# Performance work log

Hardware: AMD Instinct MI355X
Metric: run time of the kernel (lower is better)

## Reference

```python
import jax, jax.numpy as jnp
import numpy as np
import math

B, S, D, H, DFF = 4, 1024, 1024, 16, 4096
DK = D // H
EPS = 1e-6


def setup_inputs() -> dict:
    key = jax.random.key(0)
    ks = jax.random.split(key, 8)
    sc = 1.0 / math.sqrt(D)
    return {
        "x": jax.random.normal(ks[0], (B, S, D), jnp.float32),
        "src_mask": jnp.ones((B, 1, 1, S), jnp.int32),
        "wq": jax.random.normal(ks[1], (D, D), jnp.float32) * sc,
        "bq": jnp.zeros((D,), jnp.float32),
        "wk": jax.random.normal(ks[2], (D, D), jnp.float32) * sc,
        "bk": jnp.zeros((D,), jnp.float32),
        "wv": jax.random.normal(ks[3], (D, D), jnp.float32) * sc,
        "bv": jnp.zeros((D,), jnp.float32),
        "wo": jax.random.normal(ks[4], (D, D), jnp.float32) * sc,
        "bo": jnp.zeros((D,), jnp.float32),
        "w1": jax.random.normal(ks[5], (D, DFF), jnp.float32) * sc,
        "b1": jnp.zeros((DFF,), jnp.float32),
        "w2": jax.random.normal(ks[6], (DFF, D), jnp.float32) * (1.0 / math.sqrt(DFF)),
        "b2": jnp.zeros((D,), jnp.float32),
        "alpha1": jnp.ones((1,), jnp.float32),
        "beta1": jnp.zeros((1,), jnp.float32),
        "alpha2": jnp.ones((1,), jnp.float32),
        "beta2": jnp.zeros((1,), jnp.float32),
    }


def layer_norm(x, alpha, beta):
    # Faithful to the custom LayerNormalization: scalar alpha/beta,
    # torch std (unbiased, ddof=1), eps added to std (not variance).
    mean = jnp.mean(x, axis=-1, keepdims=True)
    std = jnp.std(x, axis=-1, keepdims=True, ddof=1)
    return alpha * (x - mean) / (std + EPS) + beta


def encoder_block(x, src_mask, wq, bq, wk, bk, wv, bv, wo, bo,
                  w1, b1, w2, b2, alpha1, beta1, alpha2, beta2):
    # --- residual 1: pre-norm self-attention (dropout = 0 / eval mode) ---
    xn = layer_norm(x, alpha1, beta1)
    q = (xn @ wq + bq).reshape(B, S, H, DK).transpose(0, 2, 1, 3)  # bhsd
    k = (xn @ wk + bk).reshape(B, S, H, DK).transpose(0, 2, 1, 3)
    v = (xn @ wv + bv).reshape(B, S, H, DK).transpose(0, 2, 1, 3)
    scores = jnp.einsum("bhqd,bhkd->bhqk", q, k) / math.sqrt(DK)
    scores = jnp.where(src_mask == 0, jnp.float32(-1e9), scores)
    attn = jax.nn.softmax(scores, axis=-1)
    ctx = jnp.einsum("bhqk,bhkd->bhqd", attn, v)
    ctx = ctx.transpose(0, 2, 1, 3).reshape(B, S, D)
    x = x + (ctx @ wo + bo)
    # --- residual 2: pre-norm feed-forward ---
    xn2 = layer_norm(x, alpha2, beta2)
    ff = jax.nn.relu(xn2 @ w1 + b1) @ w2 + b2
    return x + ff


def reference(x, src_mask, wq, bq, wk, bk, wv, bv, wo, bo,
              w1, b1, w2, b2, alpha1, beta1, alpha2, beta2):
    return encoder_block(x, src_mask, wq, bq, wk, bk, wv, bv, wo, bo,
                         w1, b1, w2, b2, alpha1, beta1, alpha2, beta2)
```

## Files before the change

kernel.cpp:

```cpp
#include <hip/hip_runtime.h>
#include <hip/hip_bf16.h>
#include <stdint.h>


typedef unsigned short u16;
typedef __attribute__((ext_vector_type(4))) float f32x4;
typedef __attribute__((ext_vector_type(8))) short bf16x8;
typedef __attribute__((ext_vector_type(4))) unsigned short u16x4;

__device__ __forceinline__ u16 f2b(float f) {
  unsigned int u = __builtin_bit_cast(unsigned int, f);
  u += 0x7FFFu + ((u >> 16) & 1u);
  return (u16)(u >> 16);
}

__device__ __forceinline__ void gload_lds16(const void* g, void* l) {
  __builtin_amdgcn_global_load_lds(
      reinterpret_cast<__attribute__((address_space(1))) void*>(
          reinterpret_cast<uintptr_t>(g)),
      reinterpret_cast<__attribute__((address_space(3))) void*>(
          reinterpret_cast<uintptr_t>(l)),
      16, 0, 0);
}

#define MFMA16(a, b, c) __builtin_amdgcn_mfma_f32_16x16x32_bf16((a), (b), (c), 0, 0, 0)

__global__ __launch_bounds__(256) void cast_transpose(
    const float* __restrict__ in, u16* __restrict__ out, int K, int N) {
  __shared__ float tile[32][33];
  const int n0 = blockIdx.x * 32, k0 = blockIdx.y * 32;
  const int tx = threadIdx.x & 31, ty = threadIdx.x >> 5;
#pragma unroll
  for (int i = 0; i < 32; i += 8)
    tile[ty + i][tx] = in[(int64_t)(k0 + ty + i) * N + (n0 + tx)];
  __syncthreads();
#pragma unroll
  for (int i = 0; i < 32; i += 8)
    out[(int64_t)(n0 + ty + i) * K + (k0 + tx)] = f2b(tile[tx][ty + i]);
}

__global__ void pack_bias(const float* __restrict__ bq, const float* __restrict__ bk,
                          const float* __restrict__ bv, float* __restrict__ out) {
  int i = blockIdx.x * 256 + threadIdx.x;
  const float* src = (i < 1024) ? bq : (i < 2048 ? bk : bv);
  out[i] = src[i & 1023];
}

__global__ __launch_bounds__(256) void transpose_v(
    const u16* __restrict__ qkv, u16* __restrict__ vt) {
  __shared__ u16 t[32][33];
  const int bh = blockIdx.z;
  const int b = bh >> 4, h = bh & 15;
  const int s0 = blockIdx.x * 32, d0 = blockIdx.y * 32;
  const int tx = threadIdx.x & 31, ty = threadIdx.x >> 5;
  const u16* src = qkv + (int64_t)(b * 1024) * 3072 + 2048 + h * 64;
#pragma unroll
  for (int i = 0; i < 32; i += 8)
    t[ty + i][tx] = src[(int64_t)(s0 + ty + i) * 3072 + d0 + tx];
  __syncthreads();
  u16* dst = vt + (int64_t)bh * 64 * 1024;
#pragma unroll
  for (int i = 0; i < 32; i += 8)
    dst[(int64_t)(d0 + ty + i) * 1024 + s0 + tx] = t[tx][ty + i];
}

__global__ __launch_bounds__(256) void layernorm_k(
    const float* __restrict__ x, const float* __restrict__ alpha,
    const float* __restrict__ beta, u16* __restrict__ out) {
  const int row = blockIdx.x;
  const float4 v = ((const float4*)(x + (int64_t)row * 1024))[threadIdx.x];
  float s = v.x + v.y + v.z + v.w;
  float sq = v.x * v.x + v.y * v.y + v.z * v.z + v.w * v.w;
#pragma unroll
  for (int off = 1; off < 64; off <<= 1) {
    s += __shfl_xor(s, off, 64);
    sq += __shfl_xor(sq, off, 64);
  }
  __shared__ float ss[4], ssq[4];
  const int wid = threadIdx.x >> 6;
  if ((threadIdx.x & 63) == 0) { ss[wid] = s; ssq[wid] = sq; }
  __syncthreads();
  s = ss[0] + ss[1] + ss[2] + ss[3];
  sq = ssq[0] + ssq[1] + ssq[2] + ssq[3];
  const float mean = s * (1.0f / 1024.0f);
  float var = (sq - 1024.0f * mean * mean) * (1.0f / 1023.0f);
  var = fmaxf(var, 0.0f);
  const float inv = alpha[0] / (sqrtf(var) + 1e-6f);
  const float bt = beta[0];
  u16x4 o;
  o[0] = f2b((v.x - mean) * inv + bt);
  o[1] = f2b((v.y - mean) * inv + bt);
  o[2] = f2b((v.z - mean) * inv + bt);
  o[3] = f2b((v.w - mean) * inv + bt);
  *(u16x4*)(out + (int64_t)row * 1024 + threadIdx.x * 4) = o;
}

template <int BN, bool OUT_BF16, bool RELU, bool RES>
__global__ __launch_bounds__(256) void gemm_bt(
    const u16* __restrict__ A, const u16* __restrict__ Bt,
    const float* __restrict__ bias, const float* __restrict__ res,
    void* __restrict__ Cout, int Ndim, int K) {
  constexpr int NF = BN / 32;
  __shared__ u16 Alds[2][128 * 32];
  __shared__ u16 Blds[2][BN * 32];
  const int tid = threadIdx.x;
  const int wid = tid >> 6, lane = tid & 63;
  int flat = blockIdx.y * gridDim.x + blockIdx.x;
  const int cpx = (gridDim.x * gridDim.y) >> 3;
  flat = (flat & 7) * cpx + (flat >> 3);
  const int bm0 = (flat / gridDim.x) * 128;
  const int bn0 = (flat % gridDim.x) * BN;
  const int wm = (wid >> 1) * 64, wn = (wid & 1) * (BN / 2);
  const int lrow = lane & 15, lg = lane >> 4;

  f32x4 acc[4][NF] = {};

  const int srow = tid >> 2, skoff = (tid & 3) * 8;
  const u16* Ag = A + (int64_t)(bm0 + srow) * K + skoff;
  const u16* Bg = Bt + (int64_t)(bn0 + srow) * K + skoff;
  const int64_t half = (int64_t)64 * K;

  auto stage = [&](int buf) {
    char* ad = (char*)&Alds[buf][0] + tid * 16;
    char* bd = (char*)&Blds[buf][0] + tid * 16;
    gload_lds16(Ag, ad);
    gload_lds16(Ag + half, ad + 4096);
    gload_lds16(Bg, bd);
    if (BN == 128) gload_lds16(Bg + half, bd + 4096);
    Ag += 32; Bg += 32;
  };

  const int nK = K >> 5;
  stage(0);
  __syncthreads();
  int cur = 0;
  for (int kt = 0; kt < nK; ++kt) {
    if (kt + 1 < nK) stage(cur ^ 1);
    bf16x8 af[4], bfr[NF];
#pragma unroll
    for (int f = 0; f < 4; ++f)
      af[f] = *(const bf16x8*)&Alds[cur][(wm + f * 16 + lrow) * 32 + lg * 8];
#pragma unroll
    for (int f = 0; f < NF; ++f)
      bfr[f] = *(const bf16x8*)&Blds[cur][(wn + f * 16 + lrow) * 32 + lg * 8];
#pragma unroll
    for (int mf = 0; mf < 4; ++mf)
#pragma unroll
      for (int nf = 0; nf < NF; ++nf)
        acc[mf][nf] = MFMA16(af[mf], bfr[nf], acc[mf][nf]);
    __syncthreads();
    cur ^= 1;
  }

#pragma unroll
  for (int mf = 0; mf < 4; ++mf) {
#pragma unroll
    for (int nf = 0; nf < NF; ++nf) {
      const int col = bn0 + wn + nf * 16 + lrow;
      const float bv = bias[col];
#pragma unroll
      for (int r = 0; r < 4; ++r) {
        const int row = bm0 + wm + mf * 16 + lg * 4 + r;
        float v = acc[mf][nf][r] + bv;
        if (RELU) v = fmaxf(v, 0.0f);
        if (RES) v += res[(int64_t)row * Ndim + col];
        if (OUT_BF16)
          ((u16*)Cout)[(int64_t)row * Ndim + col] = f2b(v);
        else
          ((float*)Cout)[(int64_t)row * Ndim + col] = v;
      }
    }
  }
}

__global__ __launch_bounds__(256) void attention_k(
    const u16* __restrict__ qkv, const u16* __restrict__ vt,
    const int* __restrict__ mask, u16* __restrict__ ctxout) {
  const int bh = blockIdx.y;
  const int b = bh >> 4, h = bh & 15;
  const int q0 = blockIdx.x * 64;
  const int tid = threadIdx.x, wid = tid >> 6, lane = tid & 63;
  const int lrow = lane & 15, lg = lane >> 4;

  __shared__ u16 Klds[64 * 64];
  __shared__ u16 Vtlds[64 * 64];
  __shared__ u16 Plds[4][16 * 68];

  const int64_t rs = 3072;
  const u16* Qb = qkv + (int64_t)(b * 1024) * rs + h * 64;
  const u16* Kb = Qb + 1024;
  const u16* Vtb = vt + (int64_t)bh * 64 * 1024;

  bf16x8 qf[2];
  {
    const u16* qp = Qb + (int64_t)(q0 + wid * 16 + lrow) * rs + lg * 8;
    qf[0] = *(const bf16x8*)qp;
    qf[1] = *(const bf16x8*)(qp + 32);
  }

  const int c0 = wid * 64 + lane, c1 = 256 + c0;
  const int r0 = c0 >> 3, r1 = c1 >> 3;
  const int gq0 = (c0 & 7) ^ (r0 & 7), gq1 = (c1 & 7) ^ (r1 & 7);
  char* KldsB0 = (char*)Klds + wid * 64 * 16;
  char* KldsB1 = (char*)Klds + (256 + wid * 64) * 16;
  char* VldsB0 = (char*)Vtlds + wid * 64 * 16;
  char* VldsB1 = (char*)Vtlds + (256 + wid * 64) * 16;
  const u16* Kg0 = Kb + (int64_t)r0 * rs + gq0 * 8;
  const u16* Kg1 = Kb + (int64_t)r1 * rs + gq1 * 8;
  const u16* Vg0 = Vtb + r0 * 1024 + gq0 * 8;
  const u16* Vg1 = Vtb + r1 * 1024 + gq1 * 8;

  float m[4], l[4];
  f32x4 ctx[4] = {};
#pragma unroll
  for (int r = 0; r < 4; ++r) { m[r] = -1e30f; l[r] = 0.0f; }

  for (int kt = 0; kt < 16; ++kt) {
    const int sk0 = kt * 64;
    __syncthreads();
    gload_lds16(Kg0 + (int64_t)sk0 * rs, KldsB0);
    gload_lds16(Kg1 + (int64_t)sk0 * rs, KldsB1);
    gload_lds16(Vg0 + sk0, VldsB0);
    gload_lds16(Vg1 + sk0, VldsB1);
    __syncthreads();

    f32x4 sa[4];
#pragma unroll
    for (int nf = 0; nf < 4; ++nf) {
      const int srow = nf * 16 + lrow;
      const char* kr = (const char*)Klds + srow * 128;
      bf16x8 kf0 = *(const bf16x8*)(kr + ((lg ^ (srow & 7)) * 16));
      bf16x8 kf1 = *(const bf16x8*)(kr + (((4 | lg) ^ (srow & 7)) * 16));
      f32x4 a = {};
      a = MFMA16(qf[0], kf0, a);
      a = MFMA16(qf[1], kf1, a);
      sa[nf] = a;
    }
#pragma unroll
    for (int nf = 0; nf < 4; ++nf) {
      const int mval = mask[b * 1024 + sk0 + nf * 16 + lrow];
#pragma unroll
      for (int r = 0; r < 4; ++r) {
        const float sv = sa[nf][r] * 0.125f;
        sa[nf][r] = (mval == 0) ? -1e9f : sv;
      }
    }
    float fac[4];
#pragma unroll
    for (int r = 0; r < 4; ++r) {
      float mx = fmaxf(fmaxf(sa[0][r], sa[1][r]), fmaxf(sa[2][r], sa[3][r]));
#pragma unroll
      for (int off = 1; off < 16; off <<= 1) mx = fmaxf(mx, __shfl_xor(mx, off, 64));
      const float mn = fmaxf(m[r], mx);
      fac[r] = __expf(m[r] - mn);
      m[r] = mn;
    }
    float rsum[4] = {0.f, 0.f, 0.f, 0.f};
    u16 pb[4][4];
#pragma unroll
    for (int nf = 0; nf < 4; ++nf)
#pragma unroll
      for (int r = 0; r < 4; ++r) {
        const float p = __expf(sa[nf][r] - m[r]);
        rsum[r] += p;
        pb[nf][r] = f2b(p);
      }
#pragma unroll
    for (int r = 0; r < 4; ++r) {
      float t = rsum[r];
#pragma unroll
      for (int off = 1; off < 16; off <<= 1) t += __shfl_xor(t, off, 64);
      l[r] = l[r] * fac[r] + t;
#pragma unroll
      for (int df = 0; df < 4; ++df) ctx[df][r] *= fac[r];
    }
    u16* P = &Plds[wid][0];
#pragma unroll
    for (int nf = 0; nf < 4; ++nf)
#pragma unroll
      for (int r = 0; r < 4; ++r)
        P[(lg * 4 + r) * 68 + nf * 16 + lrow] = pb[nf][r];
    bf16x8 pf0 = *(const bf16x8*)&P[lrow * 68 + lg * 8];
    bf16x8 pf1 = *(const bf16x8*)&P[lrow * 68 + 32 + lg * 8];
#pragma unroll
    for (int df = 0; df < 4; ++df) {
      const int drow = df * 16 + lrow;
      const char* vr = (const char*)Vtlds + drow * 128;
      bf16x8 vf0 = *(const bf16x8*)(vr + ((lg ^ (drow & 7)) * 16));
      bf16x8 vf1 = *(const bf16x8*)(vr + (((4 | lg) ^ (drow & 7)) * 16));
      ctx[df] = MFMA16(pf0, vf0, ctx[df]);
      ctx[df] = MFMA16(pf1, vf1, ctx[df]);
    }
  }
#pragma unroll
  for (int df = 0; df < 4; ++df)
#pragma unroll
    for (int r = 0; r < 4; ++r) {
      const int row = b * 1024 + q0 + wid * 16 + lg * 4 + r;
      const int col = h * 64 + df * 16 + lrow;
      ctxout[(int64_t)row * 1024 + col] = f2b(ctx[df][r] / l[r]);
    }
}

extern "C" void kernel_launch(void* const* d_in, const int* in_sizes, int n_in,
                              void* d_out, int out_size, void* d_ws, size_t ws_size,
                              hipStream_t stream) {
  (void)in_sizes; (void)n_in; (void)out_size; (void)ws_size;
  const float* x      = (const float*)d_in[0];
  const int*   mask   = (const int*)d_in[1];
  const float* wq     = (const float*)d_in[2];
  const float* bq     = (const float*)d_in[3];
  const float* wk     = (const float*)d_in[4];
  const float* bk     = (const float*)d_in[5];
  const float* wv     = (const float*)d_in[6];
  const float* bv     = (const float*)d_in[7];
  const float* wo     = (const float*)d_in[8];
  const float* bo     = (const float*)d_in[9];
  const float* w1     = (const float*)d_in[10];
  const float* b1     = (const float*)d_in[11];
  const float* w2     = (const float*)d_in[12];
  const float* b2     = (const float*)d_in[13];
  const float* alpha1 = (const float*)d_in[14];
  const float* beta1  = (const float*)d_in[15];
  const float* alpha2 = (const float*)d_in[16];
  const float* beta2  = (const float*)d_in[17];
  float* out = (float*)d_out;

  char* ws = (char*)d_ws;
  u16*   wqkvT = (u16*)ws;                 ws += (size_t)3072 * 1024 * 2;
  u16*   woT   = (u16*)ws;                 ws += (size_t)1024 * 1024 * 2;
  u16*   w1T   = (u16*)ws;                 ws += (size_t)4096 * 1024 * 2;
  u16*   w2T   = (u16*)ws;                 ws += (size_t)1024 * 4096 * 2;
  float* bqkv  = (float*)ws;               ws += 16384;
  u16*   xn    = (u16*)ws;                 ws += (size_t)4096 * 1024 * 2;
  u16*   qkv   = (u16*)ws;                 ws += (size_t)4096 * 3072 * 2;
  u16*   ctx   = (u16*)ws;                 ws += (size_t)4096 * 1024 * 2;
  float* x2    = (float*)ws;               ws += (size_t)4096 * 1024 * 4;
  u16*   vtb   = (u16*)ws;                 ws += (size_t)64 * 64 * 1024 * 2;
  u16*   hbuf  = qkv;

  const dim3 blk(256);
  cast_transpose<<<dim3(32, 32), blk, 0, stream>>>(wq, wqkvT, 1024, 1024);
  cast_transpose<<<dim3(32, 32), blk, 0, stream>>>(wk, wqkvT + 1024 * 1024, 1024, 1024);
  cast_transpose<<<dim3(32, 32), blk, 0, stream>>>(wv, wqkvT + 2048 * 1024, 1024, 1024);
  cast_transpose<<<dim3(32, 32), blk, 0, stream>>>(wo, woT, 1024, 1024);
  cast_transpose<<<dim3(128, 32), blk, 0, stream>>>(w1, w1T, 1024, 4096);
  cast_transpose<<<dim3(32, 128), blk, 0, stream>>>(w2, w2T, 4096, 1024);
  pack_bias<<<dim3(12), blk, 0, stream>>>(bq, bk, bv, bqkv);
  layernorm_k<<<4096, blk, 0, stream>>>(x, alpha1, beta1, xn);
  gemm_bt<128, true, false, false><<<dim3(24, 32), blk, 0, stream>>>(
      xn, wqkvT, bqkv, nullptr, qkv, 3072, 1024);
  transpose_v<<<dim3(32, 2, 64), blk, 0, stream>>>(qkv, vtb);
  attention_k<<<dim3(16, 64), blk, 0, stream>>>(qkv, vtb, mask, ctx);
  gemm_bt<64, false, false, true><<<dim3(16, 32), blk, 0, stream>>>(
      ctx, woT, bo, x, x2, 1024, 1024);
  layernorm_k<<<4096, blk, 0, stream>>>(x2, alpha2, beta2, xn);
  gemm_bt<128, true, true, false><<<dim3(32, 32), blk, 0, stream>>>(
      xn, w1T, b1, nullptr, hbuf, 4096, 1024);
  gemm_bt<64, false, false, true><<<dim3(16, 32), blk, 0, stream>>>(
      hbuf, w2T, b2, x2, out, 1024, 4096);
}
```

Measured before the change: 385.6 us.

## Double-buffer K/V in attention, fold Q scale into QKV GEMM, lazy softmax rescale

```diff
diff --git a/kernel.cpp b/kernel.cpp
--- a/kernel.cpp
+++ b/kernel.cpp
@@ -95,7 +95,7 @@
   *(u16x4*)(out + (int64_t)row * 1024 + threadIdx.x * 4) = o;
 }
 
-template <int BN, bool OUT_BF16, bool RELU, bool RES>
+template <int BN, bool OUT_BF16, bool RELU, bool RES, bool QSCALE = false>
 __global__ __launch_bounds__(256) void gemm_bt(
     const u16* __restrict__ A, const u16* __restrict__ Bt,
     const float* __restrict__ bias, const float* __restrict__ res,
@@ -162,6 +162,7 @@
       for (int r = 0; r < 4; ++r) {
         const int row = bm0 + wm + mf * 16 + lg * 4 + r;
         float v = acc[mf][nf][r] + bv;
+        if (QSCALE && col < 1024) v *= 0.125f;
         if (RELU) v = fmaxf(v, 0.0f);
         if (RES) v += res[(int64_t)row * Ndim + col];
         if (OUT_BF16)
@@ -176,14 +177,16 @@
 __global__ __launch_bounds__(256) void attention_k(
     const u16* __restrict__ qkv, const u16* __restrict__ vt,
     const int* __restrict__ mask, u16* __restrict__ ctxout) {
-  const int bh = blockIdx.y;
+  int flat = blockIdx.y * gridDim.x + blockIdx.x;
+  flat = (flat & 7) * 128 + (flat >> 3);
+  const int bh = flat >> 4;
+  const int q0 = (flat & 15) * 64;
   const int b = bh >> 4, h = bh & 15;
-  const int q0 = blockIdx.x * 64;
   const int tid = threadIdx.x, wid = tid >> 6, lane = tid & 63;
   const int lrow = lane & 15, lg = lane >> 4;
 
-  __shared__ u16 Klds[64 * 64];
-  __shared__ u16 Vtlds[64 * 64];
+  __shared__ u16 Klds[2][64 * 64];
+  __shared__ u16 Vtlds[2][64 * 64];
   __shared__ u16 Plds[4][16 * 68];
 
   const int64_t rs = 3072;
@@ -201,10 +204,6 @@
   const int c0 = wid * 64 + lane, c1 = 256 + c0;
   const int r0 = c0 >> 3, r1 = c1 >> 3;
   const int gq0 = (c0 & 7) ^ (r0 & 7), gq1 = (c1 & 7) ^ (r1 & 7);
-  char* KldsB0 = (char*)Klds + wid * 64 * 16;
-  char* KldsB1 = (char*)Klds + (256 + wid * 64) * 16;
-  char* VldsB0 = (char*)Vtlds + wid * 64 * 16;
-  char* VldsB1 = (char*)Vtlds + (256 + wid * 64) * 16;
   const u16* Kg0 = Kb + (int64_t)r0 * rs + gq0 * 8;
   const u16* Kg1 = Kb + (int64_t)r1 * rs + gq1 * 8;
   const u16* Vg0 = Vtb + r0 * 1024 + gq0 * 8;
@@ -215,20 +214,30 @@
 #pragma unroll
   for (int r = 0; r < 4; ++r) { m[r] = -1e30f; l[r] = 0.0f; }
 
+  auto stageKV = [&](int buf, int kt) {
+    const int sk0 = kt * 64;
+    char* kd = (char*)&Klds[buf][0] + wid * 1024;
+    char* vd = (char*)&Vtlds[buf][0] + wid * 1024;
+    gload_lds16(Kg0 + (int64_t)sk0 * rs, kd);
+    gload_lds16(Kg1 + (int64_t)sk0 * rs, kd + 4096);
+    gload_lds16(Vg0 + sk0, vd);
+    gload_lds16(Vg1 + sk0, vd + 4096);
+  };
+
+  stageKV(0, 0);
+  __syncthreads();
+  int cur = 0;
   for (int kt = 0; kt < 16; ++kt) {
+    if (kt + 1 < 16) stageKV(cur ^ 1, kt + 1);
+    const u16* Kc = &Klds[cur][0];
+    const u16* Vc = &Vtlds[cur][0];
     const int sk0 = kt * 64;
-    __syncthreads();
-    gload_lds16(Kg0 + (int64_t)sk0 * rs, KldsB0);
-    gload_lds16(Kg1 + (int64_t)sk0 * rs, KldsB1);
-    gload_lds16(Vg0 + sk0, VldsB0);
-    gload_lds16(Vg1 + sk0, VldsB1);
-    __syncthreads();
 
     f32x4 sa[4];
 #pragma unroll
     for (int nf = 0; nf < 4; ++nf) {
       const int srow = nf * 16 + lrow;
-      const char* kr = (const char*)Klds + srow * 128;
+      const char* kr = (const char*)Kc + srow * 128;
       bf16x8 kf0 = *(const bf16x8*)(kr + ((lg ^ (srow & 7)) * 16));
       bf16x8 kf1 = *(const bf16x8*)(kr + (((4 | lg) ^ (srow & 7)) * 16));
       f32x4 a = {};
@@ -240,20 +249,30 @@
     for (int nf = 0; nf < 4; ++nf) {
       const int mval = mask[b * 1024 + sk0 + nf * 16 + lrow];
 #pragma unroll
-      for (int r = 0; r < 4; ++r) {
-        const float sv = sa[nf][r] * 0.125f;
-        sa[nf][r] = (mval == 0) ? -1e9f : sv;
-      }
-    }
-    float fac[4];
+      for (int r = 0; r < 4; ++r)
+        sa[nf][r] = (mval == 0) ? -1e9f : sa[nf][r];
+    }
+    float mxs[4];
 #pragma unroll
     for (int r = 0; r < 4; ++r) {
       float mx = fmaxf(fmaxf(sa[0][r], sa[1][r]), fmaxf(sa[2][r], sa[3][r]));
 #pragma unroll
       for (int off = 1; off < 16; off <<= 1) mx = fmaxf(mx, __shfl_xor(mx, off, 64));
-      const float mn = fmaxf(m[r], mx);
-      fac[r] = __expf(m[r] - mn);
-      m[r] = mn;
+      mxs[r] = mx;
+    }
+    float growth = mxs[0] - m[0];
+#pragma unroll
+    for (int r = 1; r < 4; ++r) growth = fmaxf(growth, mxs[r] - m[r]);
+    if (!__all(growth <= 8.0f)) {
+#pragma unroll
+      for (int r = 0; r < 4; ++r) {
+        const float mn = fmaxf(m[r], mxs[r]);
+        const float fac = __expf(m[r] - mn);
+        m[r] = mn;
+        l[r] *= fac;
+#pragma unroll
+        for (int df = 0; df < 4; ++df) ctx[df][r] *= fac;
+      }
     }
     float rsum[4] = {0.f, 0.f, 0.f, 0.f};
     u16 pb[4][4];
@@ -270,9 +289,7 @@
       float t = rsum[r];
 #pragma unroll
       for (int off = 1; off < 16; off <<= 1) t += __shfl_xor(t, off, 64);
-      l[r] = l[r] * fac[r] + t;
-#pragma unroll
-      for (int df = 0; df < 4; ++df) ctx[df][r] *= fac[r];
+      l[r] += t;
     }
     u16* P = &Plds[wid][0];
 #pragma unroll
@@ -285,12 +302,14 @@
 #pragma unroll
     for (int df = 0; df < 4; ++df) {
       const int drow = df * 16 + lrow;
-      const char* vr = (const char*)Vtlds + drow * 128;
+      const char* vr = (const char*)Vc + drow * 128;
       bf16x8 vf0 = *(const bf16x8*)(vr + ((lg ^ (drow & 7)) * 16));
       bf16x8 vf1 = *(const bf16x8*)(vr + (((4 | lg) ^ (drow & 7)) * 16));
       ctx[df] = MFMA16(pf0, vf0, ctx[df]);
       ctx[df] = MFMA16(pf1, vf1, ctx[df]);
     }
+    __syncthreads();
+    cur ^= 1;
   }
 #pragma unroll
   for (int df = 0; df < 4; ++df)
@@ -348,7 +367,7 @@
   cast_transpose<<<dim3(32, 128), blk, 0, stream>>>(w2, w2T, 4096, 1024);
   pack_bias<<<dim3(12), blk, 0, stream>>>(bq, bk, bv, bqkv);
   layernorm_k<<<4096, blk, 0, stream>>>(x, alpha1, beta1, xn);
-  gemm_bt<128, true, false, false><<<dim3(24, 32), blk, 0, stream>>>(
+  gemm_bt<128, true, false, false, true><<<dim3(24, 32), blk, 0, stream>>>(
       xn, wqkvT, bqkv, nullptr, qkv, 3072, 1024);
   transpose_v<<<dim3(32, 2, 64), blk, 0, stream>>>(qkv, vtb);
   attention_k<<<dim3(16, 64), blk, 0, stream>>>(qkv, vtb, mask, ctx);
```

New measurement: 392.8 us. No clear change (+1.9%).
